# Kernel tuning notes

Hardware: AMD Instinct MI355X
Metric: run time of the kernel (lower is better)

The kernel has to match this reference:

```python
import jax, jax.numpy as jnp
import numpy as np

N_CODES = 8192
CODE_DIM = 256


def setup_inputs() -> dict:
    key = jax.random.key(0)
    kx, ke = jax.random.split(key)
    x = jax.random.normal(kx, (16, 4096, CODE_DIM), dtype=jnp.float32)
    # nn.Embedding weight initialized uniform(-1/n, 1/n)
    emb = jax.random.uniform(ke, (N_CODES, CODE_DIM), dtype=jnp.float32,
                             minval=-1.0 / N_CODES, maxval=1.0 / N_CODES)
    return {"x": x, "emb": emb}


def reference(x, emb):
    B, T, D = x.shape
    flat = x.reshape(-1, D)                                   # [BT, D]
    # squared euclidean distance: ||f||^2 - 2 f.e^T + ||e||^2  -> [BT, N]
    dist = ((flat * flat).sum(axis=1, keepdims=True)
            - 2.0 * flat @ emb.T
            + (emb * emb).sum(axis=1))
    idx = jnp.argmin(dist, axis=1)                            # [BT] int
    quant = emb[idx].reshape(x.shape)                         # [B, T, D]
    # commitment-style loss: mse(stop_grad(quant), x)
    loss = jnp.mean(jnp.square(jax.lax.stop_gradient(quant) - x))
    # straight-through estimator
    y = x + jax.lax.stop_gradient(quant - x)
    return y, idx.reshape(B, T), loss
```

## Files before the change

kernel.cpp:

```cpp
#include <hip/hip_runtime.h>
#include <stdint.h>


#define NCODES 8192
#define DDIM   256
#define BT     65536

#define TM     128
#define TN     128
#define NSEG   256
#define F4S    17

#define CAPC   48
#define MARGIN 7e-4f
#define CHUNKS 64
#define KSCALE 1048576.0f
#define KOFF   131072.0f
#define KMARG  737

typedef float  f32x4  __attribute__((ext_vector_type(4)));
typedef __bf16 bf16x8 __attribute__((ext_vector_type(8)));

#define GLDS16(g, l) __builtin_amdgcn_global_load_lds(                         \
    (const __attribute__((address_space(1))) void*)(g),                        \
    (__attribute__((address_space(3))) void*)(l), 16, 0, 0)
#define GLDS4(g, l) __builtin_amdgcn_global_load_lds(                          \
    (const __attribute__((address_space(1))) void*)(g),                        \
    (__attribute__((address_space(3))) void*)(l), 4, 0, 0)

__device__ __forceinline__ unsigned int fenc(float f) {
  unsigned int u = __float_as_uint(f);
  return (u & 0x80000000u) ? ~u : (u | 0x80000000u);
}
__device__ __forceinline__ float fdec(unsigned int u) {
  unsigned int v = (u & 0x80000000u) ? (u ^ 0x80000000u) : ~u;
  return __uint_as_float(v);
}

__device__ __forceinline__ float np_pairwise256_sq(const float4* __restrict__ row) {
#pragma clang fp contract(off)
  float half[2];
  #pragma unroll
  for (int h = 0; h < 2; h++) {
    float r0,r1,r2,r3,r4,r5,r6,r7;
    float4 q0 = row[h*32 + 0];
    float4 q1 = row[h*32 + 1];
    r0 = q0.x*q0.x; r1 = q0.y*q0.y; r2 = q0.z*q0.z; r3 = q0.w*q0.w;
    r4 = q1.x*q1.x; r5 = q1.y*q1.y; r6 = q1.z*q1.z; r7 = q1.w*q1.w;
    #pragma unroll
    for (int g = 1; g < 16; g++) {
      q0 = row[h*32 + g*2];
      q1 = row[h*32 + g*2 + 1];
      r0 += q0.x*q0.x; r1 += q0.y*q0.y; r2 += q0.z*q0.z; r3 += q0.w*q0.w;
      r4 += q1.x*q1.x; r5 += q1.y*q1.y; r6 += q1.z*q1.z; r7 += q1.w*q1.w;
    }
    half[h] = ((r0+r1) + (r2+r3)) + ((r4+r5) + (r6+r7));
  }
  return half[0] + half[1];
}

__device__ __forceinline__ float exact_score(const float* __restrict__ xr,
                                             const float4* __restrict__ er,
                                             float Ar, float Cv) {
#pragma clang fp contract(off)
  float b = 0.0f;
  #pragma unroll 8
  for (int q = 0; q < 64; ++q) {
    float4 ev = er[q];
    b = fmaf(xr[q * 4 + 0], ev.x, b);
    b = fmaf(xr[q * 4 + 1], ev.y, b);
    b = fmaf(xr[q * 4 + 2], ev.z, b);
    b = fmaf(xr[q * 4 + 3], ev.w, b);
  }
  const float t1 = fmaf(-2.0f, b, Ar);
  return t1 + Cv;
}

__device__ __forceinline__ void exact_score2(const float* __restrict__ xr,
                                             const float4* __restrict__ e1,
                                             const float4* __restrict__ e2,
                                             float Ar, float Cv1, float Cv2,
                                             float& s1, float& s2) {
#pragma clang fp contract(off)
  float b1 = 0.0f, b2 = 0.0f;
  #pragma unroll 8
  for (int q = 0; q < 64; ++q) {
    const float4 v1 = e1[q], v2 = e2[q];
    const float x0 = xr[q * 4 + 0], x1 = xr[q * 4 + 1];
    const float x2 = xr[q * 4 + 2], x3 = xr[q * 4 + 3];
    b1 = fmaf(x0, v1.x, b1); b2 = fmaf(x0, v2.x, b2);
    b1 = fmaf(x1, v1.y, b1); b2 = fmaf(x1, v2.y, b2);
    b1 = fmaf(x2, v1.z, b1); b2 = fmaf(x2, v2.z, b2);
    b1 = fmaf(x3, v1.w, b1); b2 = fmaf(x3, v2.w, b2);
  }
  s1 = fmaf(-2.0f, b1, Ar) + Cv1;
  s2 = fmaf(-2.0f, b2, Ar) + Cv2;
}

__global__ void vq_pre_a(const float* __restrict__ x, float* __restrict__ Astage) {
  const int t = blockIdx.x * 256 + threadIdx.x;
  Astage[t] = np_pairwise256_sq((const float4*)(x + (size_t)t * DDIM));
}

__global__ void vq_pre_c(const float* __restrict__ emb, float* __restrict__ Cws) {
  const int c = blockIdx.x * 256 + threadIdx.x;
  Cws[c] = np_pairwise256_sq((const float4*)(emb + (size_t)c * DDIM));
}

__global__ void vq_init(float* __restrict__ oloss) { *oloss = 0.0f; }

__global__ void vq_pre_e(const float* __restrict__ emb, uint4* __restrict__ ebf) {
  const int g   = blockIdx.x * 256 + threadIdx.x;
  const int c   = g >> 5;
  const int blk = g & 31;
  const float4* e4 = (const float4*)(emb + (size_t)c * DDIM);
  float4 f0 = e4[blk*2], f1 = e4[blk*2 + 1];
  union { unsigned short us[8]; uint4 v; } pk;
  pk.us[0] = __builtin_bit_cast(unsigned short, (__bf16)f0.x);
  pk.us[1] = __builtin_bit_cast(unsigned short, (__bf16)f0.y);
  pk.us[2] = __builtin_bit_cast(unsigned short, (__bf16)f0.z);
  pk.us[3] = __builtin_bit_cast(unsigned short, (__bf16)f0.w);
  pk.us[4] = __builtin_bit_cast(unsigned short, (__bf16)f1.x);
  pk.us[5] = __builtin_bit_cast(unsigned short, (__bf16)f1.y);
  pk.us[6] = __builtin_bit_cast(unsigned short, (__bf16)f1.z);
  pk.us[7] = __builtin_bit_cast(unsigned short, (__bf16)f1.w);
  ebf[(size_t)c * 32 + (blk ^ (c & 7))] = pk.v;
}

__device__ __forceinline__ void stage_chunk(const char* __restrict__ ebf,
                                            const float* __restrict__ Cws,
                                            int ch, char* ebuf_dst,
                                            float* cs_dst, int tid) {
  const char* src = ebf + (size_t)ch * 65536 + (size_t)tid * 16;
  char* dst = ebuf_dst + (size_t)tid * 16;
  #pragma unroll
  for (int i = 0; i < 8; ++i) GLDS16(src + i * 8192, dst + i * 8192);
  if (tid < 128)
    GLDS4((const char*)Cws + (size_t)ch * 512 + (size_t)tid * 4,
          (char*)cs_dst + (size_t)tid * 4);
}

__global__ __launch_bounds__(512, 2)
void vq_filter(const float* __restrict__ x, const char* __restrict__ ebf,
               const float* __restrict__ Cws, int* __restrict__ cntG,
               int* __restrict__ candG) {
  __shared__ __align__(16) char ebuf[2][65536];
  __shared__ float Cs[2][128];
  __shared__ unsigned int umin[256];
  __shared__ int cntL[256];

  const int tid  = threadIdx.x;
  const int lane = tid & 63;
  const int wid  = tid >> 6;
  const int wm   = wid >> 2;
  const int wn   = wid & 3;
  const int l15  = lane & 15;
  const int lhi  = lane >> 4;
  const int tok0 = blockIdx.x * 256;

  if (tid < 256) { umin[tid] = 0xFFFFFFFFu; cntL[tid] = 0; }

  stage_chunk(ebf, Cws, 0, ebuf[0], Cs[0], tid);

  const float4* x4 = (const float4*)x;
  bf16x8 xb[4][8];
  #pragma unroll
  for (int n = 0; n < 4; ++n) {
    const size_t trow = (size_t)(tok0 + wn * 64 + n * 16 + l15) * 64;
    #pragma unroll
    for (int kk = 0; kk < 8; ++kk) {
      float4 f0 = x4[trow + kk * 8 + lhi * 2];
      float4 f1 = x4[trow + kk * 8 + lhi * 2 + 1];
      bf16x8 v;
      v[0] = (__bf16)f0.x; v[1] = (__bf16)f0.y; v[2] = (__bf16)f0.z; v[3] = (__bf16)f0.w;
      v[4] = (__bf16)f1.x; v[5] = (__bf16)f1.y; v[6] = (__bf16)f1.z; v[7] = (__bf16)f1.w;
      xb[n][kk] = v;
    }
  }
  __syncthreads();

  const f32x4 zf = {0.f, 0.f, 0.f, 0.f};
  float rmin[4] = {1e30f, 1e30f, 1e30f, 1e30f};

  for (int c = 0; c < CHUNKS; ++c) {
    stage_chunk(ebf, Cws, (c + 1) & 63, ebuf[(c + 1) & 1], Cs[(c + 1) & 1], tid);

    const char* ecur = ebuf[c & 1];
    f32x4 acc[4][4];
    #pragma unroll
    for (int kk = 0; kk < 8; ++kk) {
      bf16x8 a[4];
      #pragma unroll
      for (int m = 0; m < 4; ++m) {
        const int row = wm * 64 + m * 16 + l15;
        const int blk = (kk * 4 + lhi) ^ (row & 7);
        a[m] = *(const bf16x8*)(ecur + row * 512 + blk * 16);
      }
      #pragma unroll
      for (int m = 0; m < 4; ++m)
        #pragma unroll
        for (int n = 0; n < 4; ++n)
          acc[m][n] = __builtin_amdgcn_mfma_f32_16x16x32_bf16(
              a[m], xb[n][kk], (kk == 0) ? zf : acc[m][n], 0, 0, 0);
    }

    const float* Csc = Cs[c & 1];
    float cvals[4][4];
    #pragma unroll
    for (int m = 0; m < 4; ++m)
      #pragma unroll
      for (int r = 0; r < 4; ++r)
        cvals[m][r] = Csc[wm * 64 + m * 16 + lhi * 4 + r];

    #pragma unroll
    for (int n = 0; n < 4; ++n) {
      const int t = wn * 64 + n * 16 + l15;
      float s[16];
      float mn = 1e30f;
      #pragma unroll
      for (int m = 0; m < 4; ++m)
        #pragma unroll
        for (int r = 0; r < 4; ++r) {
          const float v = fmaf(-2.0f, acc[m][n][r], cvals[m][r]);
          s[m * 4 + r] = v;
          mn = fminf(mn, v);
        }
      mn = fminf(mn, __shfl_xor(mn, 16));
      mn = fminf(mn, __shfl_xor(mn, 32));
      if (mn < rmin[n]) {
        rmin[n] = mn;
        if (lhi == 0) atomicMin(&umin[t], fenc(mn));
      }
      const float thr = fminf(rmin[n], fdec(umin[t])) + MARGIN;
      #pragma unroll
      for (int m = 0; m < 4; ++m)
        #pragma unroll
        for (int r = 0; r < 4; ++r) {
          if (s[m * 4 + r] <= thr) {
            const int code = c * 128 + wm * 64 + m * 16 + lhi * 4 + r;
            const int key  = (int)fmaf(s[m * 4 + r], KSCALE, KOFF);
            const int pos  = atomicAdd(&cntL[t], 1);
            if (pos < CAPC)
              candG[(size_t)(tok0 + t) * CAPC + pos] = (key << 13) | code;
          }
        }
    }

    __syncthreads();
  }

  if (tid < 256) cntG[tok0 + tid] = cntL[tid];
}

__global__ __launch_bounds__(256, 2)
void vq_rescore(const float* __restrict__ x, const float* __restrict__ emb,
                const float* __restrict__ Cws, const int* __restrict__ cntG,
                const int* __restrict__ candG, float* __restrict__ y,
                float* __restrict__ oidx, float* __restrict__ oloss) {
  __shared__ float xs[64 * 257];
  __shared__ float As[64];
  __shared__ int   idx_sh[64];
  __shared__ float red[4];
  __shared__ float rbv[256];
  __shared__ int   rbi[256];
  __shared__ int   ovf_list[64];
  __shared__ int   n_ovf;

  const int tid  = threadIdx.x;
  const int tok0 = blockIdx.x * 64;
  const float4* x4g = (const float4*)x;
  const float4* e4g = (const float4*)emb;

  if (tid == 0) n_ovf = 0;
  #pragma unroll
  for (int i = 0; i < 16; ++i) {
    const int g = tid + 256 * i, row = g >> 6, c4 = g & 63;
    float4 v = x4g[(size_t)(tok0 + row) * 64 + c4];
    float* p = &xs[row * 257 + c4 * 4];
    p[0] = v.x; p[1] = v.y; p[2] = v.z; p[3] = v.w;
  }
  if (tid < 64) As[tid] = oidx[tok0 + tid];
  __syncthreads();

  const int t  = tid >> 2;
  const int j0 = tid & 3;
  const int gt = tok0 + t;
  const int cnt = cntG[gt];
  const float* xr = &xs[t * 257];
  const float  Ar = As[t];

  if (cnt <= CAPC) {
    int pmin = 0x7FFFFFFF;
    for (int j = j0; j < cnt; j += 4) pmin = min(pmin, candG[(size_t)gt * CAPC + j]);
    pmin = min(pmin, __shfl_xor(pmin, 1));
    pmin = min(pmin, __shfl_xor(pmin, 2));
    const int thrk = (pmin >> 13) + KMARG;
    float best = 1e30f; int bid = 0x7FFFFFFF;
    for (int j = j0; j < cnt; j += 4) {
      const int e = candG[(size_t)gt * CAPC + j];
      if ((e >> 13) <= thrk) {
        const int c = e & 8191;
        const float s = exact_score(xr, e4g + (size_t)c * 64, Ar, Cws[c]);
        if (s < best || (s == best && c < bid)) { best = s; bid = c; }
      }
    }
    #pragma unroll
    for (int off = 1; off <= 2; off <<= 1) {
      const float ob = __shfl_xor(best, off);
      const int   oi = __shfl_xor(bid, off);
      if (ob < best || (ob == best && oi < bid)) { best = ob; bid = oi; }
    }
    if (j0 == 0) { idx_sh[t] = bid; oidx[gt] = (float)(bid + 1); }
  } else if (j0 == 0) {
    const int p = atomicAdd(&n_ovf, 1);
    ovf_list[p] = t;
  }
  __syncthreads();

  for (int o = 0; o < n_ovf; ++o) {
    const int tt  = ovf_list[o];
    const float* xrr = &xs[tt * 257];
    const float  At  = As[tt];
    float bv = 1e30f; int bi2 = 0x7FFFFFFF;
    for (int c0 = tid; c0 < NCODES; c0 += 512) {
      const int c1 = c0 + 256;
      float s1, s2;
      exact_score2(xrr, e4g + (size_t)c0 * 64, e4g + (size_t)c1 * 64,
                   At, Cws[c0], Cws[c1], s1, s2);
      if (s1 < bv || (s1 == bv && c0 < bi2)) { bv = s1; bi2 = c0; }
      if (s2 < bv || (s2 == bv && c1 < bi2)) { bv = s2; bi2 = c1; }
    }
    rbv[tid] = bv; rbi[tid] = bi2;
    __syncthreads();
    #pragma unroll
    for (int sft = 128; sft; sft >>= 1) {
      if (tid < sft) {
        const float v2 = rbv[tid + sft]; const int i2 = rbi[tid + sft];
        if (v2 < rbv[tid] || (v2 == rbv[tid] && i2 < rbi[tid])) {
          rbv[tid] = v2; rbi[tid] = i2;
        }
      }
      __syncthreads();
    }
    if (tid == 0) { idx_sh[tt] = rbi[0]; oidx[tok0 + tt] = (float)(rbi[0] + 1); }
    __syncthreads();
  }
  __syncthreads();

  float lsum = 0.0f;
  float4* y4 = (float4*)y;
  #pragma unroll
  for (int r = 0; r < 16; ++r) {
    const int g = tid + 256 * r, row = g >> 6, c4 = g & 63;
    const float4 ev = e4g[(size_t)idx_sh[row] * 64 + c4];
    const float4 xv = x4g[(size_t)(tok0 + row) * 64 + c4];
    y4[(size_t)(tok0 + row) * 64 + c4] = ev;
    const float dx = ev.x - xv.x, dy = ev.y - xv.y, dz = ev.z - xv.z, dw = ev.w - xv.w;
    lsum += dx * dx + dy * dy + dz * dz + dw * dw;
  }
  #pragma unroll
  for (int off = 32; off; off >>= 1) lsum += __shfl_down(lsum, off);
  if ((tid & 63) == 0) red[tid >> 6] = lsum;
  __syncthreads();
  if (tid == 0) atomicAdd(oloss, red[0] + red[1] + red[2] + red[3]);
}

__global__ void vq_fin(float* __restrict__ oloss) {
  *oloss = *oloss * (1.0f / 16777216.0f);
}

__global__ __launch_bounds__(256, 2)
void vq_main(const float* __restrict__ x, const float* __restrict__ emb,
             const float* __restrict__ Cws, float* __restrict__ y,
             float* __restrict__ oidx, float* __restrict__ oloss) {
  __shared__ float4 xs4[TM * F4S];
  __shared__ float4 es4[TN * F4S];
  __shared__ float  Cs[TN];
  __shared__ int    idx_sh[TM];
  __shared__ float  red[4];

  const int tid = threadIdx.x;
  const int ry = tid >> 4;
  const int rx = tid & 15;
  const int tok0 = blockIdx.x * TM;

  const float4* x4g = (const float4*)x;
  const float4* e4g = (const float4*)emb;

  float A_reg[8];
  #pragma unroll
  for (int m = 0; m < 8; m++) A_reg[m] = oidx[tok0 + ry + 16 * m];

  float best[8];
  int   i1[8];
  #pragma unroll
  for (int m = 0; m < 8; m++) { best[m] = 1e30f; i1[m] = 0; }

  float acc[8][8];

  for (int seg = 0; seg < NSEG; ++seg) {
    const int chunk = seg >> 2;
    const int kq = seg & 3;
    __syncthreads();
    #pragma unroll
    for (int h = 0; h < 2; h++) {
      float4 t[4];
      #pragma unroll
      for (int q = 0; q < 4; q++) {
        const int r = h * 4 + q;
        t[q] = x4g[(size_t)(tok0 + ry + 16 * r) * 64 + kq * 16 + rx];
      }
      #pragma unroll
      for (int q = 0; q < 4; q++) {
        const int r = h * 4 + q;
        xs4[(ry + 16 * r) * F4S + rx] = t[q];
      }
    }
    #pragma unroll
    for (int h = 0; h < 2; h++) {
      float4 t[4];
      #pragma unroll
      for (int q = 0; q < 4; q++) {
        const int r = h * 4 + q;
        t[q] = e4g[(size_t)(chunk * TN + ry + 16 * r) * 64 + kq * 16 + rx];
      }
      #pragma unroll
      for (int q = 0; q < 4; q++) {
        const int r = h * 4 + q;
        es4[(ry + 16 * r) * F4S + rx] = t[q];
      }
    }
    if (kq == 0 && tid < TN) Cs[tid] = Cws[chunk * TN + tid];
    __syncthreads();

    if (kq == 0) {
      #pragma unroll
      for (int m = 0; m < 8; m++)
        #pragma unroll
        for (int n = 0; n < 8; n++) acc[m][n] = 0.0f;
    }

    #pragma unroll
    for (int k4 = 0; k4 < 16; k4++) {
      float4 a[8], b[8];
      #pragma unroll
      for (int m = 0; m < 8; m++) a[m] = xs4[(ry + 16 * m) * F4S + k4];
      #pragma unroll
      for (int n = 0; n < 8; n++) b[n] = es4[(rx + 16 * n) * F4S + k4];
      #pragma unroll
      for (int m = 0; m < 8; m++)
        #pragma unroll
        for (int n = 0; n < 8; n++) {
          acc[m][n] = fmaf(a[m].x, b[n].x, acc[m][n]);
          acc[m][n] = fmaf(a[m].y, b[n].y, acc[m][n]);
          acc[m][n] = fmaf(a[m].z, b[n].z, acc[m][n]);
          acc[m][n] = fmaf(a[m].w, b[n].w, acc[m][n]);
        }
    }

    if (kq == 3) {
      const int c0 = chunk * TN;
      #pragma unroll
      for (int n = 0; n < 8; n++) {
        const float Cv = Cs[rx + 16 * n];
        const int c = c0 + rx + 16 * n;
        #pragma unroll
        for (int m = 0; m < 8; m++) {
          const float t1 = fmaf(-2.0f, acc[m][n], A_reg[m]);
          const float t2 = t1 + Cv;
          if (t2 < best[m]) { best[m] = t2; i1[m] = c; }
        }
      }
    }
  }

  __syncthreads();
  float* bv1 = (float*)xs4;
  int*   bi  = (int*)es4;
  #pragma unroll
  for (int m = 0; m < 8; m++) {
    bv1[(ry + 16 * m) * 16 + rx] = best[m];
    bi [(ry + 16 * m) * 16 + rx] = i1[m];
  }
  __syncthreads();
  if (tid < TM) {
    float v = bv1[tid * 16];
    int   id = bi[tid * 16];
    for (int t = 1; t < 16; t++) {
      const float vv = bv1[tid * 16 + t];
      const int   ii = bi [tid * 16 + t];
      if (vv < v || (vv == v && ii < id)) { v = vv; id = ii; }
    }
    idx_sh[tid] = id;
    oidx[tok0 + tid] = (float)(id + 1);
  }
  __syncthreads();

  float lsum = 0.0f;
  float4* y4 = (float4*)y;
  #pragma unroll
  for (int r = 0; r < 32; r++) {
    const int g = tid + 256 * r, row = g >> 6, c4 = g & 63;
    const float4 ev = e4g[(size_t)idx_sh[row] * 64 + c4];
    const float4 xv = x4g[(size_t)(tok0 + row) * 64 + c4];
    y4[(size_t)(tok0 + row) * 64 + c4] = ev;
    const float dx = ev.x - xv.x, dy = ev.y - xv.y, dz = ev.z - xv.z, dw = ev.w - xv.w;
    lsum += dx * dx + dy * dy + dz * dz + dw * dw;
  }
  #pragma unroll
  for (int off = 32; off; off >>= 1) lsum += __shfl_down(lsum, off);
  if ((tid & 63) == 0) red[tid >> 6] = lsum;
  __syncthreads();
  if (tid == 0) atomicAdd(oloss, red[0] + red[1] + red[2] + red[3]);
}

extern "C" void kernel_launch(void* const* d_in, const int* in_sizes, int n_in,
                              void* d_out, int out_size, void* d_ws, size_t ws_size,
                              hipStream_t stream) {
  const float* x   = (const float*)d_in[0];
  const float* emb = (const float*)d_in[1];

  float* y     = (float*)d_out;
  float* oidx  = y + (size_t)BT * DDIM;
  float* oloss = oidx + BT;

  char*  wsB   = (char*)d_ws;
  float* Cws   = (float*)wsB;
  int*   cntG  = (int*)(wsB + 32768);
  char*  ebf   = wsB + 32768 + 262144;
  int*   candG = (int*)(wsB + 294912 + 4194304);
  const size_t NEED = 294912 + 4194304 + (size_t)BT * CAPC * 4;

  vq_init <<<1, 1,           0, stream>>>(oloss);
  vq_pre_a<<<BT / 256, 256,  0, stream>>>(x, oidx);
  vq_pre_c<<<NCODES/256,256, 0, stream>>>(emb, Cws);

  if (ws_size >= NEED) {
    vq_pre_e  <<<1024, 256, 0, stream>>>(emb, (uint4*)ebf);
    vq_filter <<<256,  512, 0, stream>>>(x, ebf, Cws, cntG, candG);
    vq_rescore<<<1024, 256, 0, stream>>>(x, emb, Cws, cntG, candG, y, oidx, oloss);
  } else {
    vq_main   <<<BT / TM, 256, 0, stream>>>(x, emb, Cws, y, oidx, oloss);
  }
  vq_fin  <<<1, 1,           0, stream>>>(oloss);
}
```

Measured before the change: 864.3 us.

## Halve filter tile to 128 tokens x 64 codes and fold row norms into rescore

The filter kernel now handles 128 tokens per block with 64-code chunks instead of 256 tokens and 128 codes. That raises the grid from 256 to 512 blocks, halves LDS per block and requests four blocks per CU, aiming for better occupancy and spread across the GPU's compute units. The separate vq_pre_a launch that computed the ||x||^2 row norms is removed from the fast path. The norms are now computed inside vq_rescore from the shared-memory copy of x, and candidate keys are clamped to a valid range. The cost is twice as many embedding chunk passes, each with less MFMA work to amortise the per-chunk barrier and staging, plus an extra barrier in rescore.

```diff
diff --git a/kernel.cpp b/kernel.cpp
--- a/kernel.cpp
+++ b/kernel.cpp
@@ -13,7 +13,9 @@
 
 #define CAPC   48
 #define MARGIN 7e-4f
-#define CHUNKS 64
+#define TOKPB  128
+#define CCODES 64
+#define CHUNKS 128
 #define KSCALE 1048576.0f
 #define KOFF   131072.0f
 #define KMARG  737
@@ -53,6 +55,26 @@
       q1 = row[h*32 + g*2 + 1];
       r0 += q0.x*q0.x; r1 += q0.y*q0.y; r2 += q0.z*q0.z; r3 += q0.w*q0.w;
       r4 += q1.x*q1.x; r5 += q1.y*q1.y; r6 += q1.z*q1.z; r7 += q1.w*q1.w;
+    }
+    half[h] = ((r0+r1) + (r2+r3)) + ((r4+r5) + (r6+r7));
+  }
+  return half[0] + half[1];
+}
+
+__device__ __forceinline__ float np_pairwise256_sq_s(const float* __restrict__ row) {
+#pragma clang fp contract(off)
+  float half[2];
+  #pragma unroll
+  for (int h = 0; h < 2; h++) {
+    const float* p = row + h * 128;
+    float r0,r1,r2,r3,r4,r5,r6,r7;
+    r0 = p[0]*p[0]; r1 = p[1]*p[1]; r2 = p[2]*p[2]; r3 = p[3]*p[3];
+    r4 = p[4]*p[4]; r5 = p[5]*p[5]; r6 = p[6]*p[6]; r7 = p[7]*p[7];
+    #pragma unroll
+    for (int g = 1; g < 16; g++) {
+      const float* q = p + g * 8;
+      r0 += q[0]*q[0]; r1 += q[1]*q[1]; r2 += q[2]*q[2]; r3 += q[3]*q[3];
+      r4 += q[4]*q[4]; r5 += q[5]*q[5]; r6 += q[6]*q[6]; r7 += q[7]*q[7];
     }
     half[h] = ((r0+r1) + (r2+r3)) + ((r4+r5) + (r6+r7));
   }
@@ -131,23 +153,23 @@
                                             const float* __restrict__ Cws,
                                             int ch, char* ebuf_dst,
                                             float* cs_dst, int tid) {
-  const char* src = ebf + (size_t)ch * 65536 + (size_t)tid * 16;
+  const char* src = ebf + (size_t)ch * 32768 + (size_t)tid * 16;
   char* dst = ebuf_dst + (size_t)tid * 16;
   #pragma unroll
-  for (int i = 0; i < 8; ++i) GLDS16(src + i * 8192, dst + i * 8192);
-  if (tid < 128)
-    GLDS4((const char*)Cws + (size_t)ch * 512 + (size_t)tid * 4,
+  for (int i = 0; i < 4; ++i) GLDS16(src + i * 8192, dst + i * 8192);
+  if (tid < 64)
+    GLDS4((const char*)Cws + (size_t)ch * 256 + (size_t)tid * 4,
           (char*)cs_dst + (size_t)tid * 4);
 }
 
-__global__ __launch_bounds__(512, 2)
+__global__ __launch_bounds__(512, 4)
 void vq_filter(const float* __restrict__ x, const char* __restrict__ ebf,
                const float* __restrict__ Cws, int* __restrict__ cntG,
                int* __restrict__ candG) {
-  __shared__ __align__(16) char ebuf[2][65536];
-  __shared__ float Cs[2][128];
-  __shared__ unsigned int umin[256];
-  __shared__ int cntL[256];
+  __shared__ __align__(16) char ebuf[2][32768];
+  __shared__ float Cs[2][64];
+  __shared__ unsigned int umin[TOKPB];
+  __shared__ int cntL[TOKPB];
 
   const int tid  = threadIdx.x;
   const int lane = tid & 63;
@@ -156,17 +178,17 @@
   const int wn   = wid & 3;
   const int l15  = lane & 15;
   const int lhi  = lane >> 4;
-  const int tok0 = blockIdx.x * 256;
-
-  if (tid < 256) { umin[tid] = 0xFFFFFFFFu; cntL[tid] = 0; }
+  const int tok0 = blockIdx.x * TOKPB;
+
+  if (tid < TOKPB) { umin[tid] = 0xFFFFFFFFu; cntL[tid] = 0; }
 
   stage_chunk(ebf, Cws, 0, ebuf[0], Cs[0], tid);
 
   const float4* x4 = (const float4*)x;
-  bf16x8 xb[4][8];
-  #pragma unroll
-  for (int n = 0; n < 4; ++n) {
-    const size_t trow = (size_t)(tok0 + wn * 64 + n * 16 + l15) * 64;
+  bf16x8 xb[2][8];
+  #pragma unroll
+  for (int n = 0; n < 2; ++n) {
+    const size_t trow = (size_t)(tok0 + wn * 32 + n * 16 + l15) * 64;
     #pragma unroll
     for (int kk = 0; kk < 8; ++kk) {
       float4 f0 = x4[trow + kk * 8 + lhi * 2];
@@ -180,45 +202,46 @@
   __syncthreads();
 
   const f32x4 zf = {0.f, 0.f, 0.f, 0.f};
-  float rmin[4] = {1e30f, 1e30f, 1e30f, 1e30f};
+  float rmin[2] = {1e30f, 1e30f};
 
   for (int c = 0; c < CHUNKS; ++c) {
-    stage_chunk(ebf, Cws, (c + 1) & 63, ebuf[(c + 1) & 1], Cs[(c + 1) & 1], tid);
+    stage_chunk(ebf, Cws, (c + 1) & (CHUNKS - 1), ebuf[(c + 1) & 1],
+                Cs[(c + 1) & 1], tid);
 
     const char* ecur = ebuf[c & 1];
-    f32x4 acc[4][4];
+    f32x4 acc[2][2];
     #pragma unroll
     for (int kk = 0; kk < 8; ++kk) {
-      bf16x8 a[4];
-      #pragma unroll
-      for (int m = 0; m < 4; ++m) {
-        const int row = wm * 64 + m * 16 + l15;
+      bf16x8 a[2];
+      #pragma unroll
+      for (int m = 0; m < 2; ++m) {
+        const int row = wm * 32 + m * 16 + l15;
         const int blk = (kk * 4 + lhi) ^ (row & 7);
         a[m] = *(const bf16x8*)(ecur + row * 512 + blk * 16);
       }
       #pragma unroll
-      for (int m = 0; m < 4; ++m)
+      for (int m = 0; m < 2; ++m)
         #pragma unroll
-        for (int n = 0; n < 4; ++n)
+        for (int n = 0; n < 2; ++n)
           acc[m][n] = __builtin_amdgcn_mfma_f32_16x16x32_bf16(
               a[m], xb[n][kk], (kk == 0) ? zf : acc[m][n], 0, 0, 0);
     }
 
     const float* Csc = Cs[c & 1];
-    float cvals[4][4];
-    #pragma unroll
-    for (int m = 0; m < 4; ++m)
+    float cvals[2][4];
+    #pragma unroll
+    for (int m = 0; m < 2; ++m)
       #pragma unroll
       for (int r = 0; r < 4; ++r)
-        cvals[m][r] = Csc[wm * 64 + m * 16 + lhi * 4 + r];
-
-    #pragma unroll
-    for (int n = 0; n < 4; ++n) {
-      const int t = wn * 64 + n * 16 + l15;
-      float s[16];
+        cvals[m][r] = Csc[wm * 32 + m * 16 + lhi * 4 + r];
+
+    #pragma unroll
+    for (int n = 0; n < 2; ++n) {
+      const int t = wn * 32 + n * 16 + l15;
+      float s[8];
       float mn = 1e30f;
       #pragma unroll
-      for (int m = 0; m < 4; ++m)
+      for (int m = 0; m < 2; ++m)
         #pragma unroll
         for (int r = 0; r < 4; ++r) {
           const float v = fmaf(-2.0f, acc[m][n][r], cvals[m][r]);
@@ -233,13 +256,14 @@
       }
       const float thr = fminf(rmin[n], fdec(umin[t])) + MARGIN;
       #pragma unroll
-      for (int m = 0; m < 4; ++m)
+      for (int m = 0; m < 2; ++m)
         #pragma unroll
         for (int r = 0; r < 4; ++r) {
           if (s[m * 4 + r] <= thr) {
-            const int code = c * 128 + wm * 64 + m * 16 + lhi * 4 + r;
-            const int key  = (int)fmaf(s[m * 4 + r], KSCALE, KOFF);
-            const int pos  = atomicAdd(&cntL[t], 1);
+            const int code = c * CCODES + wm * 32 + m * 16 + lhi * 4 + r;
+            int key = (int)fmaf(s[m * 4 + r], KSCALE, KOFF);
+            key = min(max(key, 0), 262143);
+            const int pos = atomicAdd(&cntL[t], 1);
             if (pos < CAPC)
               candG[(size_t)(tok0 + t) * CAPC + pos] = (key << 13) | code;
           }
@@ -249,7 +273,7 @@
     __syncthreads();
   }
 
-  if (tid < 256) cntG[tok0 + tid] = cntL[tid];
+  if (tid < TOKPB) cntG[tok0 + tid] = cntL[tid];
 }
 
 __global__ __launch_bounds__(256, 2)
@@ -279,7 +303,8 @@
     float* p = &xs[row * 257 + c4 * 4];
     p[0] = v.x; p[1] = v.y; p[2] = v.z; p[3] = v.w;
   }
-  if (tid < 64) As[tid] = oidx[tok0 + tid];
+  __syncthreads();
+  if (tid < 64) As[tid] = np_pairwise256_sq_s(&xs[tid * 257]);
   __syncthreads();
 
   const int t  = tid >> 2;
@@ -532,15 +557,15 @@
   const size_t NEED = 294912 + 4194304 + (size_t)BT * CAPC * 4;
 
   vq_init <<<1, 1,           0, stream>>>(oloss);
-  vq_pre_a<<<BT / 256, 256,  0, stream>>>(x, oidx);
   vq_pre_c<<<NCODES/256,256, 0, stream>>>(emb, Cws);
 
   if (ws_size >= NEED) {
     vq_pre_e  <<<1024, 256, 0, stream>>>(emb, (uint4*)ebf);
-    vq_filter <<<256,  512, 0, stream>>>(x, ebf, Cws, cntG, candG);
+    vq_filter <<<BT/TOKPB, 512, 0, stream>>>(x, ebf, Cws, cntG, candG);
     vq_rescore<<<1024, 256, 0, stream>>>(x, emb, Cws, cntG, candG, y, oidx, oloss);
   } else {
-    vq_main   <<<BT / TM, 256, 0, stream>>>(x, emb, Cws, y, oidx, oloss);
+    vq_pre_a<<<BT / 256, 256, 0, stream>>>(x, oidx);
+    vq_main <<<BT / TM, 256,  0, stream>>>(x, emb, Cws, y, oidx, oloss);
   }
   vq_fin  <<<1, 1,           0, stream>>>(oloss);
 }
```

Measured after the change: 769.6 us. -11.0%, faster.
